# Kernel optimization log

Measured on AMD Instinct MI355X. Metric: run time of the kernel, lower is better.

The kernel has to match this reference:

```python
import jax, jax.numpy as jnp
import numpy as np

N = 25000        # nodes
E = 400000       # edges (before self-loops)
HEADS = 8
GROUPS = 8
F_IN = 256
HID = 64
N_CLASS = 32
N_LAYERS = 3


def grouped_linear(x, w, b):
    # x: [..., Cin], w: [G, Cin//G, Cout//G], b: [Cout]
    G = w.shape[0]
    xs = x.reshape(x.shape[:-1] + (G, -1))
    out = jnp.einsum('...gi,gio->...go', xs, w)
    return out.reshape(x.shape[:-1] + (-1,)) + b


def gcn_norm(edge_index, n):
    # PyG gcn_norm with add_self_loops=True, unit edge weights
    row = jnp.concatenate([edge_index[0], jnp.arange(n)])
    col = jnp.concatenate([edge_index[1], jnp.arange(n)])
    w = jnp.ones(row.shape[0], jnp.float32)
    deg = jax.ops.segment_sum(w, col, num_segments=n)
    dis = jnp.where(deg > 0, jax.lax.rsqrt(deg), 0.0)
    return row, col, dis[row] * w * dis[col]


def dna_conv(x_all, row, col, norm, wq, bq, wk, bk, wv, bv):
    # x_all: [N, L, H]; row/col/norm: [E'] (edges incl. self-loops)
    Ee = row.shape[0]
    L, H = x_all.shape[1], x_all.shape[2]
    dh = H // HEADS
    # query from target's latest state, key/value from full source history
    q = grouped_linear(x_all[col, -1:], wq, bq).reshape(Ee, 1, HEADS, dh).transpose(0, 2, 1, 3)
    k = grouped_linear(x_all[row], wk, bk).reshape(Ee, L, HEADS, dh).transpose(0, 2, 1, 3)
    v = grouped_linear(x_all[row], wv, bv).reshape(Ee, L, HEADS, dh).transpose(0, 2, 1, 3)
    attn = jax.nn.softmax(jnp.einsum('ehqd,ehld->ehql', q, k) / jnp.sqrt(jnp.float32(dh)), axis=-1)
    out = jnp.einsum('ehql,ehld->ehqd', attn, v)           # [E', HEADS, 1, dh]
    out = out.transpose(0, 2, 1, 3).reshape(Ee, H)          # [E', H]
    return jax.ops.segment_sum(norm[:, None] * out, col, num_segments=N)


def setup_inputs() -> dict:
    key = jax.random.key(0)
    ks = jax.random.split(key, 12)
    s = 0.2
    return {
        'x': jax.random.normal(ks[0], (N, F_IN), jnp.float32),
        'edge_index': jax.random.randint(ks[1], (2, E), 0, N),
        'lin1_w': jax.random.normal(ks[2], (F_IN, HID), jnp.float32) * 0.05,
        'lin1_b': jnp.zeros((HID,), jnp.float32),
        'wq': jax.random.normal(ks[3], (N_LAYERS, GROUPS, HID // GROUPS, HID // GROUPS), jnp.float32) * s,
        'bq': jnp.zeros((N_LAYERS, HID), jnp.float32),
        'wk': jax.random.normal(ks[4], (N_LAYERS, GROUPS, HID // GROUPS, HID // GROUPS), jnp.float32) * s,
        'bk': jnp.zeros((N_LAYERS, HID), jnp.float32),
        'wv': jax.random.normal(ks[5], (N_LAYERS, GROUPS, HID // GROUPS, HID // GROUPS), jnp.float32) * s,
        'bv': jnp.zeros((N_LAYERS, HID), jnp.float32),
        'lin2_w': jax.random.normal(ks[6], (HID, N_CLASS), jnp.float32) * 0.1,
        'lin2_b': jnp.zeros((N_CLASS,), jnp.float32),
    }


def reference(x, edge_index, lin1_w, lin1_b, wq, bq, wk, bk, wv, bv, lin2_w, lin2_b):
    row, col, norm = gcn_norm(edge_index, N)
    h = jax.nn.relu(x @ lin1_w + lin1_b)                    # [N, HID]; dropout = identity (eval)
    x_all = h[:, None, :]                                   # [N, 1, HID]
    for l in range(N_LAYERS):
        out = jax.nn.relu(dna_conv(x_all, row, col, norm,
                                   wq[l], bq[l], wk[l], bk[l], wv[l], bv[l]))
        x_all = jnp.concatenate([x_all, out[:, None, :]], axis=1)
    logits = x_all[:, -1] @ lin2_w + lin2_b                 # [N, N_CLASS]
    return jax.nn.log_softmax(logits, axis=1)
```

## Files before the change

### kernel.cpp

```cpp
#include <hip/hip_runtime.h>
#include <hip/hip_fp16.h>
#include <math.h>

#define NN 25000
#define NE 400000
#define HID 64
#define F_IN 256
#define N_CLASS 32
#define MAXL 4
#define KVS 3
#define WPAD 264
#define SCAN_NB 98

typedef _Float16 f16;
typedef _Float16 f16x2 __attribute__((ext_vector_type(2)));
typedef _Float16 f16x8 __attribute__((ext_vector_type(8)));
typedef float f32x4 __attribute__((ext_vector_type(4)));

union F16x8 {
    f16x8 v;
    f16x2 h[4];
    __half2 hh[4];
};

__device__ __forceinline__ float dot2(f16x2 a, f16x2 b, float c) {
#if __has_builtin(__builtin_amdgcn_fdot2)
    return __builtin_amdgcn_fdot2(a, b, c, false);
#else
    return c + (float)a[0] * (float)b[0] + (float)a[1] * (float)b[1];
#endif
}

__global__ void deg_kernel(const int* __restrict__ col, int* __restrict__ deg, int E) {
    int e = blockIdx.x * blockDim.x + threadIdx.x;
    if (e < E) atomicAdd(&deg[col[e]], 1);
}

__global__ void scanA_kernel(const int* __restrict__ deg, int* __restrict__ bsum, int n) {
    int t = threadIdx.x;
    int i = blockIdx.x * 256 + t;
    int v = (i < n) ? deg[i] : 0;
    #pragma unroll
    for (int off = 1; off < 64; off <<= 1) v += __shfl_xor(v, off);
    __shared__ int wsum[4];
    if ((t & 63) == 0) wsum[t >> 6] = v;
    __syncthreads();
    if (t == 0) bsum[blockIdx.x] = wsum[0] + wsum[1] + wsum[2] + wsum[3];
}

__global__ void scanC_kernel(const int* __restrict__ deg, const int* __restrict__ bsum,
                             int* __restrict__ rowptr, int* __restrict__ cursor,
                             float* __restrict__ dis, int n) {
    __shared__ int s[128];
    int t = threadIdx.x;
    {
        int v = (t < SCAN_NB) ? bsum[t] : 0;
        s[t] = v;
        __syncthreads();
        for (int off = 1; off < 128; off <<= 1) {
            int u = (t >= off) ? s[t - off] : 0;
            __syncthreads();
            s[t] += u;
            __syncthreads();
        }
    }
    int base = (blockIdx.x > 0) ? s[blockIdx.x - 1] : 0;
    __syncthreads();

    int i = blockIdx.x * 256 + t;
    int lane = t & 63, w = t >> 6;
    int v = (i < n) ? deg[i] : 0;
    int x = v;
    #pragma unroll
    for (int off = 1; off < 64; off <<= 1) {
        int u = __shfl_up(x, off);
        if (lane >= off) x += u;
    }
    __shared__ int wsum[4];
    if (lane == 63) wsum[w] = x;
    __syncthreads();
    for (int ww = 0; ww < w; ++ww) base += wsum[ww];
    if (i < n) {
        int excl = base + x - v;
        rowptr[i] = excl;
        cursor[i] = excl;
        dis[i] = rsqrtf((float)(v + 1));
    }
}

__global__ void scatter_kernel(const int* __restrict__ row, const int* __restrict__ col,
                               int* __restrict__ cursor, int* __restrict__ csr_src, int E) {
    int e = blockIdx.x * blockDim.x + threadIdx.x;
    if (e >= E) return;
    int c = col[e];
    int p = atomicAdd(&cursor[c], 1);
    csr_src[p] = row[e];
}

__global__ void wprep_kernel(const float* __restrict__ w, f16* __restrict__ wt) {
    int e = blockIdx.x * blockDim.x + threadIdx.x;
    int k = e >> 6, nn = e & 63;
    wt[nn * F_IN + k] = (f16)w[e];
}

__global__ void __launch_bounds__(256) lin1_mfma_kernel(
        const float* __restrict__ x, const f16x8* __restrict__ wt,
        const float* __restrict__ b, float* __restrict__ x_all, int n) {
    __shared__ f16 wlds[64 * WPAD];
    int t = threadIdx.x;
    #pragma unroll
    for (int j = 0; j < 8; ++j) {
        int idx = t + j * 256;
        int e = idx * 8;
        int nr = e >> 8, k0 = e & 255;
        *(f16x8*)&wlds[nr * WPAD + k0] = wt[idx];
    }
    __syncthreads();
    int wave = t >> 6, lane = t & 63;
    int m = lane & 15, quad = lane >> 4;
    int rowA = blockIdx.x * 64 + wave * 16 + m;
    int rA = min(rowA, n - 1);
    const float* xp = x + (size_t)rA * F_IN + quad * 8;
    f32x4 acc[4] = {};
    for (int kk = 0; kk < F_IN; kk += 32) {
        float4 x0 = *(const float4*)(xp + kk);
        float4 x1 = *(const float4*)(xp + kk + 4);
        f16x8 a;
        a[0] = (f16)x0.x; a[1] = (f16)x0.y; a[2] = (f16)x0.z; a[3] = (f16)x0.w;
        a[4] = (f16)x1.x; a[5] = (f16)x1.y; a[6] = (f16)x1.z; a[7] = (f16)x1.w;
        #pragma unroll
        for (int nt = 0; nt < 4; ++nt) {
            f16x8 bf = *(const f16x8*)&wlds[(nt * 16 + m) * WPAD + kk + quad * 8];
            acc[nt] = __builtin_amdgcn_mfma_f32_16x16x32_f16(a, bf, acc[nt], 0, 0, 0);
        }
    }
    int rowC = blockIdx.x * 64 + wave * 16 + quad * 4;
    #pragma unroll
    for (int nt = 0; nt < 4; ++nt) {
        int col = nt * 16 + m;
        float bias = b[col];
        #pragma unroll
        for (int r = 0; r < 4; ++r) {
            int row = rowC + r;
            if (row < n)
                x_all[(size_t)row * (MAXL * HID) + col] = fmaxf(acc[nt][r] + bias, 0.f);
        }
    }
}

__global__ void transform1_kernel(const float* __restrict__ x_all,
                                  const float* __restrict__ wv, const float* __restrict__ bv,
                                  const float* __restrict__ dis,
                                  f16x2* __restrict__ KV, int n) {
    int t = blockIdx.x * blockDim.x + threadIdx.x;
    int node = t >> 5, u = t & 31;
    if (node >= n) return;
    int g = u >> 2;
    int o0 = (u & 3) * 2;
    const float4* xg4 = (const float4*)(x_all + (size_t)node * (MAXL * HID) + g * 8);
    float4 xa = xg4[0], xb = xg4[1];
    float xv[8] = {xa.x, xa.y, xa.z, xa.w, xb.x, xb.y, xb.z, xb.w};
    float d = dis[node];
    const float* wgv = wv + g * 64;
    float v0 = bv[g * 8 + o0], v1 = bv[g * 8 + o0 + 1];
    #pragma unroll
    for (int i = 0; i < 8; ++i) {
        v0 = fmaf(xv[i], wgv[i * 8 + o0], v0);
        v1 = fmaf(xv[i], wgv[i * 8 + o0 + 1], v1);
    }
    f16x2 vh; vh[0] = (f16)(v0 * d); vh[1] = (f16)(v1 * d);
    KV[((size_t)node * KVS * 2 + 1) * 32 + u] = vh;
}

__global__ void gather1_kernel(const int* __restrict__ rowptr, const int* __restrict__ deg,
                               const int* __restrict__ csr_src, const float* __restrict__ dis,
                               const f16x8* __restrict__ KV8, float* __restrict__ x_all, int n) {
    int wave = (int)((blockIdx.x * (size_t)blockDim.x + threadIdx.x) >> 6);
    int lane = threadIdx.x & 63;
    if (wave >= n) return;
    int c = wave;
    int u = lane & 7;
    int slot = lane >> 3;
    float nc = dis[c];
    int beg = rowptr[c];
    int dc = deg[c] + 1;
    float acc[8];
    #pragma unroll
    for (int i = 0; i < 8; ++i) acc[i] = 0.f;

    for (int j = 0; j < dc; j += 32) {
        int jj0 = j + slot, jj1 = jj0 + 8, jj2 = jj0 + 16, jj3 = jj0 + 24;
        bool va0 = jj0 < dc, va1 = jj1 < dc, va2 = jj2 < dc, va3 = jj3 < dc;
        int r0 = c, r1 = c, r2 = c, r3 = c;
        if (va0 && jj0 > 0) r0 = csr_src[beg + jj0 - 1];
        if (va1)            r1 = csr_src[beg + jj1 - 1];
        if (va2)            r2 = csr_src[beg + jj2 - 1];
        if (va3)            r3 = csr_src[beg + jj3 - 1];
        F16x8 v0, v1, v2, v3;
        v0.v = KV8[(size_t)r0 * (KVS * 2 * 8) + 8 + u];
        v1.v = KV8[(size_t)r1 * (KVS * 2 * 8) + 8 + u];
        v2.v = KV8[(size_t)r2 * (KVS * 2 * 8) + 8 + u];
        v3.v = KV8[(size_t)r3 * (KVS * 2 * 8) + 8 + u];
        __half2 p0 = __float2half2_rn(va0 ? 1.f : 0.f);
        __half2 p1 = __float2half2_rn(va1 ? 1.f : 0.f);
        __half2 p2 = __float2half2_rn(va2 ? 1.f : 0.f);
        __half2 p3 = __float2half2_rn(va3 ? 1.f : 0.f);
        __half2 ha[4];
        #pragma unroll
        for (int i2 = 0; i2 < 4; ++i2) {
            ha[i2] = __hmul2(p0, v0.hh[i2]);
            ha[i2] = __hfma2(p1, v1.hh[i2], ha[i2]);
            ha[i2] = __hfma2(p2, v2.hh[i2], ha[i2]);
            ha[i2] = __hfma2(p3, v3.hh[i2], ha[i2]);
        }
        #pragma unroll
        for (int i2 = 0; i2 < 4; ++i2) {
            float2 f = __half22float2(ha[i2]);
            acc[i2 * 2]     += f.x;
            acc[i2 * 2 + 1] += f.y;
        }
    }
    #pragma unroll
    for (int off = 8; off < 64; off <<= 1) {
        #pragma unroll
        for (int i = 0; i < 8; ++i) acc[i] += __shfl_xor(acc[i], off);
    }
    if (slot == 0) {
        float4* dst = (float4*)(x_all + ((size_t)c * MAXL + 1) * HID + u * 8);
        dst[0] = make_float4(fmaxf(acc[0] * nc, 0.f), fmaxf(acc[1] * nc, 0.f),
                             fmaxf(acc[2] * nc, 0.f), fmaxf(acc[3] * nc, 0.f));
        dst[1] = make_float4(fmaxf(acc[4] * nc, 0.f), fmaxf(acc[5] * nc, 0.f),
                             fmaxf(acc[6] * nc, 0.f), fmaxf(acc[7] * nc, 0.f));
    }
}

__global__ void transform_kernel(const float* __restrict__ x_all,
                                 const float* __restrict__ wq, const float* __restrict__ bq,
                                 const float* __restrict__ wk, const float* __restrict__ bk,
                                 const float* __restrict__ wv, const float* __restrict__ bv,
                                 const float* __restrict__ dis,
                                 f16x2* __restrict__ Q2, f16x2* __restrict__ KV,
                                 int n, int L) {
    int t = blockIdx.x * blockDim.x + threadIdx.x;
    int node = t >> 5, u = t & 31;
    if (node >= n) return;
    int g = u >> 2;
    int o0 = (u & 3) * 2;
    const float* xrow = x_all + (size_t)node * (MAXL * HID);
    float d = dis[node];

    {
        const float4* xg4 = (const float4*)(xrow + (L - 1) * HID + g * 8);
        float4 xa = xg4[0], xb = xg4[1];
        float xv[8] = {xa.x, xa.y, xa.z, xa.w, xb.x, xb.y, xb.z, xb.w};
        const float* wg = wq + g * 64;
        float a0 = bq[g * 8 + o0], a1 = bq[g * 8 + o0 + 1];
        #pragma unroll
        for (int i = 0; i < 8; ++i) {
            a0 = fmaf(xv[i], wg[i * 8 + o0], a0);
            a1 = fmaf(xv[i], wg[i * 8 + o0 + 1], a1);
        }
        f16x2 q; q[0] = (f16)a0; q[1] = (f16)a1;
        Q2[(size_t)node * 32 + u] = q;
    }
    for (int ll = 0; ll < L; ++ll) {
        const float4* xg4 = (const float4*)(xrow + ll * HID + g * 8);
        float4 xa = xg4[0], xb = xg4[1];
        float xv[8] = {xa.x, xa.y, xa.z, xa.w, xb.x, xb.y, xb.z, xb.w};
        const float* wgk = wk + g * 64;
        const float* wgv = wv + g * 64;
        float k0 = bk[g * 8 + o0], k1 = bk[g * 8 + o0 + 1];
        float v0 = bv[g * 8 + o0], v1 = bv[g * 8 + o0 + 1];
        #pragma unroll
        for (int i = 0; i < 8; ++i) {
            k0 = fmaf(xv[i], wgk[i * 8 + o0], k0);
            k1 = fmaf(xv[i], wgk[i * 8 + o0 + 1], k1);
            v0 = fmaf(xv[i], wgv[i * 8 + o0], v0);
            v1 = fmaf(xv[i], wgv[i * 8 + o0 + 1], v1);
        }
        f16x2 kh; kh[0] = (f16)k0; kh[1] = (f16)k1;
        f16x2 vh; vh[0] = (f16)(v0 * d); vh[1] = (f16)(v1 * d);
        size_t base = ((size_t)node * KVS + ll) * 2;
        KV[(base + 0) * 32 + u] = kh;
        KV[(base + 1) * 32 + u] = vh;
    }
}

template <int L>
__global__ void gather_kernel(const int* __restrict__ rowptr, const int* __restrict__ deg,
                              const int* __restrict__ csr_src, const float* __restrict__ dis,
                              const f16x8* __restrict__ Q8, const f16x8* __restrict__ KV8,
                              float* __restrict__ x_all, int n) {
    int wave = (int)((blockIdx.x * (size_t)blockDim.x + threadIdx.x) >> 6);
    int lane = threadIdx.x & 63;
    if (wave >= n) return;
    int c = wave;
    int u = lane & 7;
    int slot = lane >> 3;
    F16x8 q; q.v = Q8[(size_t)c * 8 + u];
    float nc = dis[c];
    int beg = rowptr[c];
    int dc = deg[c] + 1;
    float acc[8];
    #pragma unroll
    for (int i = 0; i < 8; ++i) acc[i] = 0.f;

    for (int j = 0; j < dc; j += 32) {
        int jj0 = j + slot;
        int jj1 = jj0 + 8;
        int jj2 = jj0 + 16;
        int jj3 = jj0 + 24;
        bool va0 = jj0 < dc, va1 = jj1 < dc, va2 = jj2 < dc, va3 = jj3 < dc;
        int r0 = c, r1 = c, r2 = c, r3 = c;
        if (va0 && jj0 > 0) r0 = csr_src[beg + jj0 - 1];
        if (va1)            r1 = csr_src[beg + jj1 - 1];
        if (va2)            r2 = csr_src[beg + jj2 - 1];
        if (va3)            r3 = csr_src[beg + jj3 - 1];

        size_t rb0 = (size_t)r0 * (KVS * 2 * 8);
        size_t rb1 = (size_t)r1 * (KVS * 2 * 8);
        size_t rb2 = (size_t)r2 * (KVS * 2 * 8);
        size_t rb3 = (size_t)r3 * (KVS * 2 * 8);
        F16x8 kk0[L], vv0[L], kk1[L], vv1[L], kk2[L], vv2[L], kk3[L], vv3[L];
        #pragma unroll
        for (int ll = 0; ll < L; ++ll) {
            kk0[ll].v = KV8[rb0 + ll * 16 + u];
            vv0[ll].v = KV8[rb0 + ll * 16 + 8 + u];
            kk1[ll].v = KV8[rb1 + ll * 16 + u];
            vv1[ll].v = KV8[rb1 + ll * 16 + 8 + u];
            kk2[ll].v = KV8[rb2 + ll * 16 + u];
            vv2[ll].v = KV8[rb2 + ll * 16 + 8 + u];
            kk3[ll].v = KV8[rb3 + ll * 16 + u];
            vv3[ll].v = KV8[rb3 + ll * 16 + 8 + u];
        }

        {
            float s0[L], s1[L];
            #pragma unroll
            for (int ll = 0; ll < L; ++ll) {
                float p0 = 0.f, p1 = 0.f;
                #pragma unroll
                for (int i2 = 0; i2 < 4; ++i2) {
                    p0 = dot2(q.h[i2], kk0[ll].h[i2], p0);
                    p1 = dot2(q.h[i2], kk1[ll].h[i2], p1);
                }
                s0[ll] = p0 * 0.35355339059327373f;
                s1[ll] = p1 * 0.35355339059327373f;
            }
            float m0 = s0[0], m1 = s1[0];
            #pragma unroll
            for (int ll = 1; ll < L; ++ll) { m0 = fmaxf(m0, s0[ll]); m1 = fmaxf(m1, s1[ll]); }
            float sum0 = 0.f, sum1 = 0.f;
            #pragma unroll
            for (int ll = 0; ll < L; ++ll) {
                s0[ll] = __expf(s0[ll] - m0); sum0 += s0[ll];
                s1[ll] = __expf(s1[ll] - m1); sum1 += s1[ll];
            }
            float inv0 = va0 ? 1.f / sum0 : 0.f;
            float inv1 = va1 ? 1.f / sum1 : 0.f;
            __half2 ha[4];
            #pragma unroll
            for (int i2 = 0; i2 < 4; ++i2) ha[i2] = __float2half2_rn(0.f);
            #pragma unroll
            for (int ll = 0; ll < L; ++ll) {
                __half2 p0 = __float2half2_rn(s0[ll] * inv0);
                __half2 p1 = __float2half2_rn(s1[ll] * inv1);
                #pragma unroll
                for (int i2 = 0; i2 < 4; ++i2) {
                    ha[i2] = __hfma2(p0, vv0[ll].hh[i2], ha[i2]);
                    ha[i2] = __hfma2(p1, vv1[ll].hh[i2], ha[i2]);
                }
            }
            #pragma unroll
            for (int i2 = 0; i2 < 4; ++i2) {
                float2 f = __half22float2(ha[i2]);
                acc[i2 * 2]     += f.x;
                acc[i2 * 2 + 1] += f.y;
            }
        }
        {
            float s0[L], s1[L];
            #pragma unroll
            for (int ll = 0; ll < L; ++ll) {
                float p0 = 0.f, p1 = 0.f;
                #pragma unroll
                for (int i2 = 0; i2 < 4; ++i2) {
                    p0 = dot2(q.h[i2], kk2[ll].h[i2], p0);
                    p1 = dot2(q.h[i2], kk3[ll].h[i2], p1);
                }
                s0[ll] = p0 * 0.35355339059327373f;
                s1[ll] = p1 * 0.35355339059327373f;
            }
            float m0 = s0[0], m1 = s1[0];
            #pragma unroll
            for (int ll = 1; ll < L; ++ll) { m0 = fmaxf(m0, s0[ll]); m1 = fmaxf(m1, s1[ll]); }
            float sum0 = 0.f, sum1 = 0.f;
            #pragma unroll
            for (int ll = 0; ll < L; ++ll) {
                s0[ll] = __expf(s0[ll] - m0); sum0 += s0[ll];
                s1[ll] = __expf(s1[ll] - m1); sum1 += s1[ll];
            }
            float inv0 = va2 ? 1.f / sum0 : 0.f;
            float inv1 = va3 ? 1.f / sum1 : 0.f;
            __half2 ha[4];
            #pragma unroll
            for (int i2 = 0; i2 < 4; ++i2) ha[i2] = __float2half2_rn(0.f);
            #pragma unroll
            for (int ll = 0; ll < L; ++ll) {
                __half2 p0 = __float2half2_rn(s0[ll] * inv0);
                __half2 p1 = __float2half2_rn(s1[ll] * inv1);
                #pragma unroll
                for (int i2 = 0; i2 < 4; ++i2) {
                    ha[i2] = __hfma2(p0, vv2[ll].hh[i2], ha[i2]);
                    ha[i2] = __hfma2(p1, vv3[ll].hh[i2], ha[i2]);
                }
            }
            #pragma unroll
            for (int i2 = 0; i2 < 4; ++i2) {
                float2 f = __half22float2(ha[i2]);
                acc[i2 * 2]     += f.x;
                acc[i2 * 2 + 1] += f.y;
            }
        }
    }
    #pragma unroll
    for (int off = 8; off < 64; off <<= 1) {
        #pragma unroll
        for (int i = 0; i < 8; ++i) acc[i] += __shfl_xor(acc[i], off);
    }
    if (slot == 0) {
        float4* dst = (float4*)(x_all + ((size_t)c * MAXL + L) * HID + u * 8);
        dst[0] = make_float4(fmaxf(acc[0] * nc, 0.f), fmaxf(acc[1] * nc, 0.f),
                             fmaxf(acc[2] * nc, 0.f), fmaxf(acc[3] * nc, 0.f));
        dst[1] = make_float4(fmaxf(acc[4] * nc, 0.f), fmaxf(acc[5] * nc, 0.f),
                             fmaxf(acc[6] * nc, 0.f), fmaxf(acc[7] * nc, 0.f));
    }
}

__global__ void final_kernel(const float* __restrict__ x_all, const float* __restrict__ w2,
                             const float* __restrict__ b2, float* __restrict__ out, int n) {
    int t = blockIdx.x * blockDim.x + threadIdx.x;
    int node = t >> 5;
    int o = t & 31;
    if (node >= n) return;
    const float* xr = x_all + (size_t)node * (MAXL * HID) + 3 * HID;
    float logit = b2[o];
    #pragma unroll
    for (int d = 0; d < HID; ++d) logit = fmaf(xr[d], w2[d * N_CLASS + o], logit);
    float m = logit;
    for (int off = 16; off; off >>= 1) m = fmaxf(m, __shfl_xor(m, off, 32));
    float e = expf(logit - m);
    float sum = e;
    for (int off = 16; off; off >>= 1) sum += __shfl_xor(sum, off, 32);
    out[(size_t)node * N_CLASS + o] = (logit - m) - logf(sum);
}

extern "C" void kernel_launch(void* const* d_in, const int* in_sizes, int n_in,
                              void* d_out, int out_size, void* d_ws, size_t ws_size,
                              hipStream_t stream) {
    const float* x      = (const float*)d_in[0];
    const int*   eidx   = (const int*)d_in[1];
    const float* lin1_w = (const float*)d_in[2];
    const float* lin1_b = (const float*)d_in[3];
    const float* wq     = (const float*)d_in[4];
    const float* bq     = (const float*)d_in[5];
    const float* wk     = (const float*)d_in[6];
    const float* bk     = (const float*)d_in[7];
    const float* wv     = (const float*)d_in[8];
    const float* bv     = (const float*)d_in[9];
    const float* lin2_w = (const float*)d_in[10];
    const float* lin2_b = (const float*)d_in[11];
    float* out = (float*)d_out;

    const int n  = NN;
    const int E  = NE;
    const int* row = eidx;
    const int* col = eidx + E;

    char* ws = (char*)d_ws;
    float*  x_all  = (float*)ws;   ws += (size_t)NN * MAXL * HID * 4;
    f16x2*  Q2     = (f16x2*)ws;   ws += (size_t)NN * 32 * 4;
    f16x2*  KV     = (f16x2*)ws;   ws += (size_t)NN * KVS * 2 * 32 * 4;
    float*  dis    = (float*)ws;   ws += (size_t)NN * 4;
    int*    deg    = (int*)ws;     ws += (size_t)NN * 4;
    int*    rowptr = (int*)ws;     ws += (size_t)NN * 4;
    int*    cursor = (int*)ws;     ws += (size_t)NN * 4;
    int*    csr    = (int*)ws;     ws += (size_t)NE * 4;
    f16*    wt16   = (f16*)ws;     ws += (size_t)HID * F_IN * 2;
    int*    bsum   = (int*)ws;     ws += 128 * 4;

    hipMemsetAsync(deg, 0, (size_t)NN * 4, stream);
    deg_kernel<<<(E + 255) / 256, 256, 0, stream>>>(col, deg, E);
    scanA_kernel<<<SCAN_NB, 256, 0, stream>>>(deg, bsum, n);
    scanC_kernel<<<SCAN_NB, 256, 0, stream>>>(deg, bsum, rowptr, cursor, dis, n);
    scatter_kernel<<<(E + 255) / 256, 256, 0, stream>>>(row, col, cursor, csr, E);
    wprep_kernel<<<(HID * F_IN + 255) / 256, 256, 0, stream>>>(lin1_w, wt16);

    lin1_mfma_kernel<<<(n + 63) / 64, 256, 0, stream>>>(x, (const f16x8*)wt16, lin1_b, x_all, n);

    int blocks = (n + 3) / 4;
    transform1_kernel<<<(n * 32 + 255) / 256, 256, 0, stream>>>(
        x_all, wv, bv, dis, KV, n);
    gather1_kernel<<<blocks, 256, 0, stream>>>(rowptr, deg, csr, dis,
                                               (const f16x8*)KV, x_all, n);

    for (int l = 1; l < 3; ++l) {
        int L = l + 1;
        transform_kernel<<<(n * 32 + 255) / 256, 256, 0, stream>>>(
            x_all, wq + l * 512, bq + l * 64, wk + l * 512, bk + l * 64,
            wv + l * 512, bv + l * 64, dis, Q2, KV, n, L);
        if (L == 2) gather_kernel<2><<<blocks, 256, 0, stream>>>(rowptr, deg, csr, dis, (const f16x8*)Q2, (const f16x8*)KV, x_all, n);
        else        gather_kernel<3><<<blocks, 256, 0, stream>>>(rowptr, deg, csr, dis, (const f16x8*)Q2, (const f16x8*)KV, x_all, n);
    }

    final_kernel<<<(n * N_CLASS + 255) / 256, 256, 0, stream>>>(x_all, lin2_w, lin2_b, out, n);
}
```

Baseline: 281.3 us.

## Merge independent kernels into combined launches and fuse final classifier into last gather

Runs the degree-count atomics and the lin1 MFMA GEMM in one launch by splitting blocks by index, and likewise runs the CSR scatter together with the first-layer value transform. The last-layer gather now computes the lin2 projection and log-softmax in registers directly from its per-node accumulator, so the separate final kernel and its reread of x_all are gone. This cuts launch count and a global round trip, and lets independent work overlap. The cost is extra shuffles in the final gather and a combined kernel that reserves LDS even for the degree blocks, which may lower occupancy there.

```diff
diff --git a/kernel.cpp b/kernel.cpp
--- a/kernel.cpp
+++ b/kernel.cpp
@@ -31,9 +31,62 @@
 #endif
 }
 
-__global__ void deg_kernel(const int* __restrict__ col, int* __restrict__ deg, int E) {
+__global__ void wprep_kernel(const float* __restrict__ w, f16* __restrict__ wt) {
     int e = blockIdx.x * blockDim.x + threadIdx.x;
-    if (e < E) atomicAdd(&deg[col[e]], 1);
+    int k = e >> 6, nn = e & 63;
+    wt[nn * F_IN + k] = (f16)w[e];
+}
+
+__global__ void __launch_bounds__(256) deg_lin1_kernel(
+        const int* __restrict__ col, int* __restrict__ deg, int E, int degBlocks,
+        const float* __restrict__ x, const f16x8* __restrict__ wt,
+        const float* __restrict__ b, float* __restrict__ x_all, int n) {
+    __shared__ f16 wlds[64 * WPAD];
+    if (blockIdx.x < degBlocks) {
+        int e = blockIdx.x * 256 + threadIdx.x;
+        if (e < E) atomicAdd(&deg[col[e]], 1);
+        return;
+    }
+    int bid = blockIdx.x - degBlocks;
+    int t = threadIdx.x;
+    #pragma unroll
+    for (int j = 0; j < 8; ++j) {
+        int idx = t + j * 256;
+        int e = idx * 8;
+        int nr = e >> 8, k0 = e & 255;
+        *(f16x8*)&wlds[nr * WPAD + k0] = wt[idx];
+    }
+    __syncthreads();
+    int wave = t >> 6, lane = t & 63;
+    int m = lane & 15, quad = lane >> 4;
+    int rowA = bid * 64 + wave * 16 + m;
+    int rA = min(rowA, n - 1);
+    const float* xp = x + (size_t)rA * F_IN + quad * 8;
+    f32x4 acc[4] = {};
+    for (int kk = 0; kk < F_IN; kk += 32) {
+        float4 x0 = *(const float4*)(xp + kk);
+        float4 x1 = *(const float4*)(xp + kk + 4);
+        f16x8 a;
+        a[0] = (f16)x0.x; a[1] = (f16)x0.y; a[2] = (f16)x0.z; a[3] = (f16)x0.w;
+        a[4] = (f16)x1.x; a[5] = (f16)x1.y; a[6] = (f16)x1.z; a[7] = (f16)x1.w;
+        #pragma unroll
+        for (int nt = 0; nt < 4; ++nt) {
+            f16x8 bf = *(const f16x8*)&wlds[(nt * 16 + m) * WPAD + kk + quad * 8];
+            acc[nt] = __builtin_amdgcn_mfma_f32_16x16x32_f16(a, bf, acc[nt], 0, 0, 0);
+        }
+    }
+    int rowC = bid * 64 + wave * 16 + quad * 4;
+    #pragma unroll
+    for (int nt = 0; nt < 4; ++nt) {
+        int c2 = nt * 16 + m;
+        float bias = b[c2];
+        #pragma unroll
+        for (int r = 0; r < 4; ++r) {
+            int row = rowC + r;
+            if (row < n)
+                x_all[(size_t)row * (MAXL * HID) + c2] = fmaxf(acc[nt][r] + bias, 0.f);
+        }
+    }
 }
 
 __global__ void scanA_kernel(const int* __restrict__ deg, int* __restrict__ bsum, int n) {
@@ -88,71 +141,22 @@
     }
 }
 
-__global__ void scatter_kernel(const int* __restrict__ row, const int* __restrict__ col,
-                               int* __restrict__ cursor, int* __restrict__ csr_src, int E) {
-    int e = blockIdx.x * blockDim.x + threadIdx.x;
-    if (e >= E) return;
-    int c = col[e];
-    int p = atomicAdd(&cursor[c], 1);
-    csr_src[p] = row[e];
-}
-
-__global__ void wprep_kernel(const float* __restrict__ w, f16* __restrict__ wt) {
-    int e = blockIdx.x * blockDim.x + threadIdx.x;
-    int k = e >> 6, nn = e & 63;
-    wt[nn * F_IN + k] = (f16)w[e];
-}
-
-__global__ void __launch_bounds__(256) lin1_mfma_kernel(
-        const float* __restrict__ x, const f16x8* __restrict__ wt,
-        const float* __restrict__ b, float* __restrict__ x_all, int n) {
-    __shared__ f16 wlds[64 * WPAD];
-    int t = threadIdx.x;
-    #pragma unroll
-    for (int j = 0; j < 8; ++j) {
-        int idx = t + j * 256;
-        int e = idx * 8;
-        int nr = e >> 8, k0 = e & 255;
-        *(f16x8*)&wlds[nr * WPAD + k0] = wt[idx];
-    }
-    __syncthreads();
-    int wave = t >> 6, lane = t & 63;
-    int m = lane & 15, quad = lane >> 4;
-    int rowA = blockIdx.x * 64 + wave * 16 + m;
-    int rA = min(rowA, n - 1);
-    const float* xp = x + (size_t)rA * F_IN + quad * 8;
-    f32x4 acc[4] = {};
-    for (int kk = 0; kk < F_IN; kk += 32) {
-        float4 x0 = *(const float4*)(xp + kk);
-        float4 x1 = *(const float4*)(xp + kk + 4);
-        f16x8 a;
-        a[0] = (f16)x0.x; a[1] = (f16)x0.y; a[2] = (f16)x0.z; a[3] = (f16)x0.w;
-        a[4] = (f16)x1.x; a[5] = (f16)x1.y; a[6] = (f16)x1.z; a[7] = (f16)x1.w;
-        #pragma unroll
-        for (int nt = 0; nt < 4; ++nt) {
-            f16x8 bf = *(const f16x8*)&wlds[(nt * 16 + m) * WPAD + kk + quad * 8];
-            acc[nt] = __builtin_amdgcn_mfma_f32_16x16x32_f16(a, bf, acc[nt], 0, 0, 0);
-        }
-    }
-    int rowC = blockIdx.x * 64 + wave * 16 + quad * 4;
-    #pragma unroll
-    for (int nt = 0; nt < 4; ++nt) {
-        int col = nt * 16 + m;
-        float bias = b[col];
-        #pragma unroll
-        for (int r = 0; r < 4; ++r) {
-            int row = rowC + r;
-            if (row < n)
-                x_all[(size_t)row * (MAXL * HID) + col] = fmaxf(acc[nt][r] + bias, 0.f);
-        }
-    }
-}
-
-__global__ void transform1_kernel(const float* __restrict__ x_all,
+__global__ void scatter_t1_kernel(const int* __restrict__ row, const int* __restrict__ col,
+                                  int* __restrict__ cursor, int* __restrict__ csr_src,
+                                  int E, int scatBlocks,
+                                  const float* __restrict__ x_all,
                                   const float* __restrict__ wv, const float* __restrict__ bv,
                                   const float* __restrict__ dis,
                                   f16x2* __restrict__ KV, int n) {
-    int t = blockIdx.x * blockDim.x + threadIdx.x;
+    if (blockIdx.x < scatBlocks) {
+        int e = blockIdx.x * 256 + threadIdx.x;
+        if (e >= E) return;
+        int c = col[e];
+        int p = atomicAdd(&cursor[c], 1);
+        csr_src[p] = row[e];
+        return;
+    }
+    int t = (blockIdx.x - scatBlocks) * 256 + threadIdx.x;
     int node = t >> 5, u = t & 31;
     if (node >= n) return;
     int g = u >> 2;
@@ -286,11 +290,13 @@
     }
 }
 
-template <int L>
+template <int L, bool FINAL>
 __global__ void gather_kernel(const int* __restrict__ rowptr, const int* __restrict__ deg,
                               const int* __restrict__ csr_src, const float* __restrict__ dis,
                               const f16x8* __restrict__ Q8, const f16x8* __restrict__ KV8,
-                              float* __restrict__ x_all, int n) {
+                              float* __restrict__ x_all,
+                              const float* __restrict__ w2, const float* __restrict__ b2,
+                              float* __restrict__ out, int n) {
     int wave = (int)((blockIdx.x * (size_t)blockDim.x + threadIdx.x) >> 6);
     int lane = threadIdx.x & 63;
     if (wave >= n) return;
@@ -428,31 +434,50 @@
         #pragma unroll
         for (int i = 0; i < 8; ++i) acc[i] += __shfl_xor(acc[i], off);
     }
-    if (slot == 0) {
-        float4* dst = (float4*)(x_all + ((size_t)c * MAXL + L) * HID + u * 8);
-        dst[0] = make_float4(fmaxf(acc[0] * nc, 0.f), fmaxf(acc[1] * nc, 0.f),
-                             fmaxf(acc[2] * nc, 0.f), fmaxf(acc[3] * nc, 0.f));
-        dst[1] = make_float4(fmaxf(acc[4] * nc, 0.f), fmaxf(acc[5] * nc, 0.f),
-                             fmaxf(acc[6] * nc, 0.f), fmaxf(acc[7] * nc, 0.f));
-    }
-}
-
-__global__ void final_kernel(const float* __restrict__ x_all, const float* __restrict__ w2,
-                             const float* __restrict__ b2, float* __restrict__ out, int n) {
-    int t = blockIdx.x * blockDim.x + threadIdx.x;
-    int node = t >> 5;
-    int o = t & 31;
-    if (node >= n) return;
-    const float* xr = x_all + (size_t)node * (MAXL * HID) + 3 * HID;
-    float logit = b2[o];
-    #pragma unroll
-    for (int d = 0; d < HID; ++d) logit = fmaf(xr[d], w2[d * N_CLASS + o], logit);
-    float m = logit;
-    for (int off = 16; off; off >>= 1) m = fmaxf(m, __shfl_xor(m, off, 32));
-    float e = expf(logit - m);
-    float sum = e;
-    for (int off = 16; off; off >>= 1) sum += __shfl_xor(sum, off, 32);
-    out[(size_t)node * N_CLASS + o] = (logit - m) - logf(sum);
+
+    if constexpr (!FINAL) {
+        if (slot == 0) {
+            float4* dst = (float4*)(x_all + ((size_t)c * MAXL + L) * HID + u * 8);
+            dst[0] = make_float4(fmaxf(acc[0] * nc, 0.f), fmaxf(acc[1] * nc, 0.f),
+                                 fmaxf(acc[2] * nc, 0.f), fmaxf(acc[3] * nc, 0.f));
+            dst[1] = make_float4(fmaxf(acc[4] * nc, 0.f), fmaxf(acc[5] * nc, 0.f),
+                                 fmaxf(acc[6] * nc, 0.f), fmaxf(acc[7] * nc, 0.f));
+        }
+    } else {
+        float xn[8];
+        #pragma unroll
+        for (int i = 0; i < 8; ++i) xn[i] = fmaxf(acc[i] * nc, 0.f);
+        float pl[4] = {0.f, 0.f, 0.f, 0.f};
+        const float* w2p = w2 + (u * 8) * N_CLASS + slot * 4;
+        #pragma unroll
+        for (int i = 0; i < 8; ++i) {
+            float4 wv4 = *(const float4*)(w2p + i * N_CLASS);
+            pl[0] = fmaf(xn[i], wv4.x, pl[0]);
+            pl[1] = fmaf(xn[i], wv4.y, pl[1]);
+            pl[2] = fmaf(xn[i], wv4.z, pl[2]);
+            pl[3] = fmaf(xn[i], wv4.w, pl[3]);
+        }
+        #pragma unroll
+        for (int off = 1; off < 8; off <<= 1) {
+            #pragma unroll
+            for (int cc = 0; cc < 4; ++cc) pl[cc] += __shfl_xor(pl[cc], off);
+        }
+        float4 bb = *(const float4*)(b2 + slot * 4);
+        pl[0] += bb.x; pl[1] += bb.y; pl[2] += bb.z; pl[3] += bb.w;
+        float lm = fmaxf(fmaxf(pl[0], pl[1]), fmaxf(pl[2], pl[3]));
+        #pragma unroll
+        for (int off = 8; off < 64; off <<= 1) lm = fmaxf(lm, __shfl_xor(lm, off));
+        float se = __expf(pl[0] - lm) + __expf(pl[1] - lm)
+                 + __expf(pl[2] - lm) + __expf(pl[3] - lm);
+        #pragma unroll
+        for (int off = 8; off < 64; off <<= 1) se += __shfl_xor(se, off);
+        float ls = logf(se);
+        if (u == 0) {
+            float4 o4 = make_float4(pl[0] - lm - ls, pl[1] - lm - ls,
+                                    pl[2] - lm - ls, pl[3] - lm - ls);
+            *(float4*)(out + (size_t)c * N_CLASS + slot * 4) = o4;
+        }
+    }
 }
 
 extern "C" void kernel_launch(void* const* d_in, const int* in_sizes, int n_in,
@@ -489,29 +514,37 @@
     f16*    wt16   = (f16*)ws;     ws += (size_t)HID * F_IN * 2;
     int*    bsum   = (int*)ws;     ws += 128 * 4;
 
+    const int degBlocks  = (E + 255) / 256;
+    const int lin1Blocks = (n + 63) / 64;
+    const int t1Blocks   = (n * 32 + 255) / 256;
+    const int blocks     = (n + 3) / 4;
+
     hipMemsetAsync(deg, 0, (size_t)NN * 4, stream);
-    deg_kernel<<<(E + 255) / 256, 256, 0, stream>>>(col, deg, E);
+    wprep_kernel<<<(HID * F_IN + 255) / 256, 256, 0, stream>>>(lin1_w, wt16);
+
+    deg_lin1_kernel<<<degBlocks + lin1Blocks, 256, 0, stream>>>(
+        col, deg, E, degBlocks, x, (const f16x8*)wt16, lin1_b, x_all, n);
+
     scanA_kernel<<<SCAN_NB, 256, 0, stream>>>(deg, bsum, n);
     scanC_kernel<<<SCAN_NB, 256, 0, stream>>>(deg, bsum, rowptr, cursor, dis, n);
-    scatter_kernel<<<(E + 255) / 256, 256, 0, stream>>>(row, col, cursor, csr, E);
-    wprep_kernel<<<(HID * F_IN + 255) / 256, 256, 0, stream>>>(lin1_w, wt16);
-
-    lin1_mfma_kernel<<<(n + 63) / 64, 256, 0, stream>>>(x, (const f16x8*)wt16, lin1_b, x_all, n);
-
-    int blocks = (n + 3) / 4;
-    transform1_kernel<<<(n * 32 + 255) / 256, 256, 0, stream>>>(
-        x_all, wv, bv, dis, KV, n);
+
+    scatter_t1_kernel<<<degBlocks + t1Blocks, 256, 0, stream>>>(
+        row, col, cursor, csr, E, degBlocks, x_all, wv, bv, dis, KV, n);
+
     gather1_kernel<<<blocks, 256, 0, stream>>>(rowptr, deg, csr, dis,
                                                (const f16x8*)KV, x_all, n);
 
-    for (int l = 1; l < 3; ++l) {
-        int L = l + 1;
-        transform_kernel<<<(n * 32 + 255) / 256, 256, 0, stream>>>(
-            x_all, wq + l * 512, bq + l * 64, wk + l * 512, bk + l * 64,
-            wv + l * 512, bv + l * 64, dis, Q2, KV, n, L);
-        if (L == 2) gather_kernel<2><<<blocks, 256, 0, stream>>>(rowptr, deg, csr, dis, (const f16x8*)Q2, (const f16x8*)KV, x_all, n);
-        else        gather_kernel<3><<<blocks, 256, 0, stream>>>(rowptr, deg, csr, dis, (const f16x8*)Q2, (const f16x8*)KV, x_all, n);
-    }
-
-    final_kernel<<<(n * N_CLASS + 255) / 256, 256, 0, stream>>>(x_all, lin2_w, lin2_b, out, n);
-}
+    transform_kernel<<<t1Blocks, 256, 0, stream>>>(
+        x_all, wq + 512, bq + 64, wk + 512, bk + 64, wv + 512, bv + 64,
+        dis, Q2, KV, n, 2);
+    gather_kernel<2, false><<<blocks, 256, 0, stream>>>(
+        rowptr, deg, csr, dis, (const f16x8*)Q2, (const f16x8*)KV,
+        x_all, lin2_w, lin2_b, out, n);
+
+    transform_kernel<<<t1Blocks, 256, 0, stream>>>(
+        x_all, wq + 1024, bq + 128, wk + 1024, bk + 128, wv + 1024, bv + 128,
+        dis, Q2, KV, n, 3);
+    gather_kernel<3, true><<<blocks, 256, 0, stream>>>(
+        rowptr, deg, csr, dis, (const f16x8*)Q2, (const f16x8*)KV,
+        x_all, lin2_w, lin2_b, out, n);
+}
```

Measured after the change: 272.8 us (median of 2 runs). 3.0% less time.
